# Optimization experiments

Hardware: AMD Instinct MI355X
Metric: run time of the kernel (lower is better)

The kernel has to match this reference:

```python
import jax, jax.numpy as jnp
import numpy as np

SEQ_LEN, BATCH, VOCAB, EMB, HID, NUM_LAYERS = 128, 64, 10000, 512, 512, 2


def setup_inputs() -> dict:
    key = jax.random.key(0)
    ks = jax.random.split(key, 16)
    b = float(np.sqrt(1.0 / HID))  # Linear init bound per init_weights_uniform
    u = lambda k, shape, bound: jax.random.uniform(k, shape, jnp.float32, -bound, bound)
    L = NUM_LAYERS - 1
    return {
        "inputs": jax.random.randint(ks[0], (SEQ_LEN, BATCH), 0, VOCAB, dtype=jnp.int32),
        "hidden": jnp.zeros((NUM_LAYERS, BATCH, HID), jnp.float32),
        "emb": u(ks[1], (VOCAB, EMB), 0.1),
        "W_ih0": u(ks[2], (HID, EMB), b),
        "b_ih0": u(ks[3], (HID,), b),
        "W_hh0": u(ks[4], (HID, HID), b),
        "b_hh0": u(ks[5], (HID,), b),
        "W_in": u(ks[6], (L, HID, HID), b),
        "b_in": u(ks[7], (L, HID), b),
        "W_hh": u(ks[8], (L, HID, HID), b),
        "b_hh": u(ks[9], (L, HID), b),
        "Wy": u(ks[10], (VOCAB, HID), 0.1),
        "by": jnp.zeros((VOCAB,), jnp.float32),
    }


def reference(inputs, hidden, emb, W_ih0, b_ih0, W_hh0, b_hh0,
              W_in, b_in, W_hh, b_hh, Wy, by):
    n_extra = W_in.shape[0]  # num_layers - 1 (static)

    def step(h, x_t):
        # h: [L, B, H]; x_t: [B] int tokens
        e = emb[x_t]  # [B, E]
        h0 = jnp.tanh(e @ W_ih0.T + b_ih0 + h[0] @ W_hh0.T + b_hh0)
        hs = [h0]
        for l in range(n_extra):  # small static layer loop
            hl = jnp.tanh(hs[-1] @ W_in[l].T + b_in[l]
                          + h[l + 1] @ W_hh[l].T + b_hh[l])
            hs.append(hl)
        h_new = jnp.stack(hs)  # [L, B, H]
        logits_t = hs[-1] @ Wy.T + by  # [B, V]
        return h_new, logits_t

    hidden_final, logits = jax.lax.scan(step, hidden, inputs)
    return logits, hidden_final  # [S, B, V], [L, B, H]
```

## Files before the change

### kernel.cpp

```cpp
#include <hip/hip_runtime.h>
#include <hip/hip_bf16.h>

#define SEQ 128
#define BAT 64
#define VOC 10000
#define EMBD 512
#define HID 512
#define BH (BAT*HID)
#define PRE0_OFF 0
#define H0_OFF   ((size_t)SEQ*BH)
#define H1_OFF   (H0_OFF + (size_t)(SEQ+1)*BH)
#define FLAGS_OFF (H1_OFF + (size_t)(SEQ+1)*BH)
#define CONV_OFF (FLAGS_OFF + 256)
#define LOGITS_N ((size_t)SEQ*BAT*VOC)
#define CONV_USHORTS 5382144ull
#define WS_NEED_FLOATS (CONV_OFF + CONV_USHORTS/2)

typedef __attribute__((ext_vector_type(8))) __bf16 bf16x8;
typedef __attribute__((ext_vector_type(4))) float f32x4;

__global__ __launch_bounds__(256) void init_state_k(const float* __restrict__ hidden,
                                                    float* __restrict__ h0_0,
                                                    float* __restrict__ h1_0,
                                                    unsigned* __restrict__ flags) {
    int i = blockIdx.x * 256 + threadIdx.x;
    if (i < 256) flags[i] = 0u;
    if (i < BH) { h0_0[i] = hidden[i]; h1_0[i] = hidden[BH + i]; }
}

__global__ __launch_bounds__(256) void gemm_nt_k(
    const float* __restrict__ A, const int* __restrict__ tok,
    const float* __restrict__ Bm,
    const float* __restrict__ bias0, const float* __restrict__ bias1,
    float* __restrict__ C, int N, int K, int ldc)
{
    __shared__ float As[32][132];
    __shared__ float Bs[32][132];
    __shared__ int toks[128];

    const int tid = threadIdx.x;
    const int r0 = blockIdx.x * 128;
    const int c0 = blockIdx.y * 128;

    if (tok != nullptr && tid < 128) toks[tid] = tok[r0 + tid];
    __syncthreads();

    const int tn = tid & 15;
    const int tm = tid >> 4;
    const int m0 = tm * 8, n0 = tn * 8;

    float acc[8][8];
#pragma unroll
    for (int i = 0; i < 8; ++i)
#pragma unroll
        for (int j = 0; j < 8; ++j) acc[i][j] = 0.f;

    for (int k0 = 0; k0 < K; k0 += 32) {
#pragma unroll
        for (int p = 0; p < 4; ++p) {
            int idx = p * 256 + tid;
            int row = idx >> 3;
            int kq  = (idx & 7) << 2;
            size_t arow = tok ? (size_t)toks[row] : (size_t)(r0 + row);
            float4 a = *(const float4*)(A + arow * (size_t)K + k0 + kq);
            As[kq+0][row] = a.x; As[kq+1][row] = a.y;
            As[kq+2][row] = a.z; As[kq+3][row] = a.w;
            int gc = c0 + row;
            float4 b = make_float4(0.f, 0.f, 0.f, 0.f);
            if (gc < N) b = *(const float4*)(Bm + (size_t)gc * K + k0 + kq);
            Bs[kq+0][row] = b.x; Bs[kq+1][row] = b.y;
            Bs[kq+2][row] = b.z; Bs[kq+3][row] = b.w;
        }
        __syncthreads();
#pragma unroll 8
        for (int k = 0; k < 32; ++k) {
            float4 a0 = *(const float4*)&As[k][m0];
            float4 a1 = *(const float4*)&As[k][m0 + 4];
            float4 b0 = *(const float4*)&Bs[k][n0];
            float4 b1 = *(const float4*)&Bs[k][n0 + 4];
            float am[8] = {a0.x,a0.y,a0.z,a0.w,a1.x,a1.y,a1.z,a1.w};
            float bn[8] = {b0.x,b0.y,b0.z,b0.w,b1.x,b1.y,b1.z,b1.w};
#pragma unroll
            for (int i = 0; i < 8; ++i)
#pragma unroll
                for (int j = 0; j < 8; ++j) acc[i][j] += am[i] * bn[j];
        }
        __syncthreads();
    }

    const bool full = (c0 + 128 <= N);
#pragma unroll
    for (int i = 0; i < 8; ++i) {
        size_t r = (size_t)(r0 + m0 + i);
        float* crow = C + r * (size_t)ldc;
#pragma unroll
        for (int j = 0; j < 8; ++j) {
            int c = c0 + n0 + j;
            if (full || c < N) {
                float v = acc[i][j];
                if (bias0) v += bias0[c];
                if (bias1) v += bias1[c];
                crow[c] = v;
            }
        }
    }
}


#define BFLY(S, N)                                                     \
    {                                                                  \
        _Pragma("unroll")                                              \
        for (int i = 0; i < N; ++i) {                                  \
            float lo_ = a[i], hi_ = a[i + N];                          \
            float send_ = (lane & S) ? lo_ : hi_;                      \
            float recv_ = __shfl_xor(send_, S);                        \
            a[i] = ((lane & S) ? hi_ : lo_) + recv_;                   \
        }                                                              \
    }

__global__ __launch_bounds__(512) void recurrence_k(
    const float* __restrict__ pre0, const float* __restrict__ W_hh0,
    const float* __restrict__ W_in, const float* __restrict__ b_in,
    const float* __restrict__ W_hh, const float* __restrict__ b_hh,
    float* __restrict__ h0_all, float* __restrict__ h1_all,
    unsigned* __restrict__ flags)
{
    __shared__ float xs[16384];

    const int tid  = threadIdx.x;
    const int lane = tid & 63;
    const int wv   = tid >> 6;
    const int p = ((lane&1)<<5)|((lane&2)<<3)|((lane&4)<<1)
                | ((lane&8)>>1)|((lane&16)>>3)|((lane&32)>>5);
    const int b_own = p >> 3, j_own = p & 7;

    unsigned* fl1 = flags;
    unsigned* fl2 = flags + 64;

    float4 wr[8][2];
    float a[64];

    if (blockIdx.x < 64) {
        const int g = blockIdx.x >> 4, jb = blockIdx.x & 15;
        const int bt = wv & 1, jt = wv >> 1;
        const size_t win = (size_t)(g << 4) * HID;
#pragma unroll
        for (int jj = 0; jj < 8; ++jj) {
            const float* wp = W_hh0 + (size_t)(jb*32 + jt*8 + jj) * HID;
            wr[jj][0] = *(const float4*)(wp + lane*4);
            wr[jj][1] = *(const float4*)(wp + 256 + lane*4);
        }
        const unsigned* grp = fl1 + (g << 4);
        unsigned* myf = fl1 + (g << 4) + jb;
        const int bg = (g << 4) + (bt << 3) + b_own;
        const int jg = jb*32 + jt*8 + j_own;

        for (unsigned t = 1; t <= SEQ; ++t) {
            float pf = pre0[(size_t)(t-1)*BH + (size_t)bg*HID + jg];
            for (;;) {
                unsigned v = __hip_atomic_load(&grp[lane & 15], __ATOMIC_RELAXED,
                                               __HIP_MEMORY_SCOPE_AGENT);
                if (__ballot(v < (t - 1)) == 0ull) break;
            }
            __syncthreads();
            {
                const float4* src = (const float4*)(h0_all + (size_t)(t-1)*BH + win);
                float4 r0_, r1_, r2_, r3_;
                asm volatile("global_load_dwordx4 %0, %1, off sc0 sc1" : "=v"(r0_) : "v"(src + tid));
                asm volatile("global_load_dwordx4 %0, %1, off sc0 sc1" : "=v"(r1_) : "v"(src + tid + 512));
                asm volatile("global_load_dwordx4 %0, %1, off sc0 sc1" : "=v"(r2_) : "v"(src + tid + 1024));
                asm volatile("global_load_dwordx4 %0, %1, off sc0 sc1" : "=v"(r3_) : "v"(src + tid + 1536));
                asm volatile("s_waitcnt vmcnt(0)" ::: "memory");
                __builtin_amdgcn_sched_barrier(0);
                float4* dst = (float4*)xs;
                dst[tid] = r0_; dst[tid+512] = r1_; dst[tid+1024] = r2_; dst[tid+1536] = r3_;
            }
            __syncthreads();
#pragma unroll
            for (int i = 0; i < 64; ++i) a[i] = 0.f;
#pragma unroll
            for (int b = 0; b < 8; ++b) {
                const int row = (bt << 3) + b;
                float4 ha = *(const float4*)&xs[row*512 + lane*4];
                float4 hb = *(const float4*)&xs[row*512 + 256 + lane*4];
#pragma unroll
                for (int jj = 0; jj < 8; ++jj) {
                    a[b*8+jj] += ha.x*wr[jj][0].x + ha.y*wr[jj][0].y
                               + ha.z*wr[jj][0].z + ha.w*wr[jj][0].w
                               + hb.x*wr[jj][1].x + hb.y*wr[jj][1].y
                               + hb.z*wr[jj][1].z + hb.w*wr[jj][1].w;
                }
            }
            BFLY(1,32) BFLY(2,16) BFLY(4,8) BFLY(8,4) BFLY(16,2) BFLY(32,1)
            float v = tanhf(a[0] + pf);
            __hip_atomic_store(&h0_all[(size_t)t*BH + (size_t)bg*HID + jg], v,
                               __ATOMIC_RELAXED, __HIP_MEMORY_SCOPE_AGENT);
            asm volatile("s_waitcnt vmcnt(0)" ::: "memory");
            __syncthreads();
            if (tid == 0) __hip_atomic_store(myf, t, __ATOMIC_RELAXED,
                                             __HIP_MEMORY_SCOPE_AGENT);
        }
    } else {
        const int idx = blockIdx.x - 64;
        const int g = idx >> 5, jb = idx & 31;
        const int bt = wv & 1, jt = (wv >> 1) & 1, kt = wv >> 2;
        const size_t win = (size_t)(g << 4) * HID;
        const float* Wmat = kt ? W_hh : W_in;
#pragma unroll
        for (int jj = 0; jj < 8; ++jj) {
            const float* wp = Wmat + (size_t)(jb*16 + jt*8 + jj) * HID;
            wr[jj][0] = *(const float4*)(wp + lane*4);
            wr[jj][1] = *(const float4*)(wp + 256 + lane*4);
        }
        const unsigned* grpA = fl1 + (g << 4);
        const unsigned* grpB = fl2 + (g << 5);
        unsigned* myf = fl2 + (g << 5) + jb;
        const int bg = (g << 4) + (bt << 3) + b_own;
        const int jg = jb*16 + jt*8 + j_own;
        const float bias = b_in[jg] + b_hh[jg];
        const int scx = (wv & 3) * 64 + lane;

        for (unsigned t = 1; t <= SEQ; ++t) {
            for (;;) {
                unsigned v1 = __hip_atomic_load(&grpA[lane & 15], __ATOMIC_RELAXED,
                                                __HIP_MEMORY_SCOPE_AGENT);
                unsigned v2 = __hip_atomic_load(&grpB[lane & 31], __ATOMIC_RELAXED,
                                                __HIP_MEMORY_SCOPE_AGENT);
                if (__ballot(v1 < t) == 0ull && __ballot(v2 < (t - 1)) == 0ull) break;
            }
            __syncthreads();
            {
                const int q = tid & 255;
                const float4* src = (tid < 256)
                    ? (const float4*)(h0_all + (size_t)t*BH + win)
                    : (const float4*)(h1_all + (size_t)(t-1)*BH + win);
                float4 rr[8];
#pragma unroll
                for (int i = 0; i < 8; ++i)
                    asm volatile("global_load_dwordx4 %0, %1, off sc0 sc1"
                                 : "=v"(rr[i]) : "v"(src + q + i*256));
                asm volatile("s_waitcnt vmcnt(0)" ::: "memory");
                __builtin_amdgcn_sched_barrier(0);
                float4* dst = (float4*)(xs + ((tid < 256) ? 0 : 8192));
#pragma unroll
                for (int i = 0; i < 8; ++i) dst[q + i*256] = rr[i];
            }
            __syncthreads();
#pragma unroll
            for (int i = 0; i < 64; ++i) a[i] = 0.f;
            const float* xsrc = xs + (kt ? 8192 : 0);
#pragma unroll
            for (int b = 0; b < 8; ++b) {
                const int row = (bt << 3) + b;
                float4 ha = *(const float4*)&xsrc[row*512 + lane*4];
                float4 hb = *(const float4*)&xsrc[row*512 + 256 + lane*4];
#pragma unroll
                for (int jj = 0; jj < 8; ++jj) {
                    a[b*8+jj] += ha.x*wr[jj][0].x + ha.y*wr[jj][0].y
                               + ha.z*wr[jj][0].z + ha.w*wr[jj][0].w
                               + hb.x*wr[jj][1].x + hb.y*wr[jj][1].y
                               + hb.z*wr[jj][1].z + hb.w*wr[jj][1].w;
                }
            }
            BFLY(1,32) BFLY(2,16) BFLY(4,8) BFLY(8,4) BFLY(16,2) BFLY(32,1)
            __syncthreads();
            if (kt) xs[scx] = a[0];
            __syncthreads();
            if (!kt) {
                float v = tanhf(a[0] + xs[scx] + bias);
                __hip_atomic_store(&h1_all[(size_t)t*BH + (size_t)bg*HID + jg], v,
                                   __ATOMIC_RELAXED, __HIP_MEMORY_SCOPE_AGENT);
            }
            asm volatile("s_waitcnt vmcnt(0)" ::: "memory");
            __syncthreads();
            if (tid == 0) __hip_atomic_store(myf, t, __ATOMIC_RELAXED,
                                             __HIP_MEMORY_SCOPE_AGENT);
        }
    }
}

__global__ __launch_bounds__(256) void copy_out_k(const float* __restrict__ h0_all,
                                                  const float* __restrict__ h1_all,
                                                  float* __restrict__ out_hidden) {
    int g = blockIdx.x * 256 + threadIdx.x;
    if (g < BH)            out_hidden[g] = h0_all[(size_t)SEQ * BH + g];
    else if (g < 2 * BH)   out_hidden[g] = h1_all[(size_t)SEQ * BH + (g - BH)];
}


__device__ __forceinline__ unsigned bf16_rne(float x) {
    unsigned u = __float_as_uint(x);
    unsigned r = u + 0x7fffu + ((u >> 16) & 1u);
    return r >> 16;
}

__global__ __launch_bounds__(256) void split_hi_k(const float* __restrict__ src,
                                                  unsigned short* __restrict__ hi,
                                                  int n4) {
    int i = blockIdx.x * 256 + threadIdx.x;
    if (i >= n4) return;
    float4 v = ((const float4*)src)[i];
    ushort4 h4;
    h4.x = (unsigned short)bf16_rne(v.x); h4.y = (unsigned short)bf16_rne(v.y);
    h4.z = (unsigned short)bf16_rne(v.z); h4.w = (unsigned short)bf16_rne(v.w);
    ((ushort4*)hi)[i] = h4;
}

__global__ __launch_bounds__(256) void gemm_mfma2f_k(
    const float* __restrict__ Ag, const int* __restrict__ tok,
    const unsigned short* __restrict__ Bhg,
    const float* __restrict__ bias0, const float* __restrict__ bias1,
    float* __restrict__ C, int N, int ldc)
{
    __shared__ __align__(16) unsigned short sAh[128*64];
    __shared__ __align__(16) unsigned short sAl[128*64];
    __shared__ __align__(16) unsigned short sBh[128*64];

    const int tid = threadIdx.x;
    const int flat = blockIdx.y * gridDim.x + blockIdx.x;
    const int cpx  = (gridDim.x * gridDim.y) >> 3;
    const int w    = (flat & 7) * cpx + (flat >> 3);
    const int r0 = (w & 63) * 128, c0 = (w >> 6) * 128;

    const int lane = tid & 63, wvv = tid >> 6;
    const int mh = wvv >> 1, nh = wvv & 1;

    f32x4 acc[4][4];
#pragma unroll
    for (int i = 0; i < 4; ++i)
#pragma unroll
        for (int j = 0; j < 4; ++j) acc[i][j] = (f32x4){0.f, 0.f, 0.f, 0.f};

    const int srow = tid >> 1, shalf = tid & 1;
    const size_t arow = tok ? (size_t)tok[r0 + srow] : (size_t)(r0 + srow);
    const size_t abase = arow * 512 + (size_t)shalf * 32;
    const int brow = c0 + srow;
    const bool bok = brow < N;
    const size_t bbase = (size_t)(bok ? brow : 0) * 512 + shalf * 32;
    const int woff = srow * 64;
    const int swz = srow & 7;

    float4 fa[4][2];
    uint4 vbh[4];
#pragma unroll
    for (int g = 0; g < 4; ++g) {
        fa[g][0] = *(const float4*)(Ag + abase + g*8);
        fa[g][1] = *(const float4*)(Ag + abase + g*8 + 4);
        vbh[g]   = bok ? *(const uint4*)(Bhg + bbase + g*8) : (uint4){0,0,0,0};
    }

    for (int k0 = 0; k0 < 512; k0 += 64) {
        __syncthreads();
#pragma unroll
        for (int g = 0; g < 4; ++g) {
            float f[8] = {fa[g][0].x, fa[g][0].y, fa[g][0].z, fa[g][0].w,
                          fa[g][1].x, fa[g][1].y, fa[g][1].z, fa[g][1].w};
            unsigned hh[8], ll[8];
#pragma unroll
            for (int q = 0; q < 8; ++q) {
                hh[q] = bf16_rne(f[q]);
                ll[q] = bf16_rne(f[q] - __uint_as_float(hh[q] << 16));
            }
            uint4 ph = { hh[0] | (hh[1]<<16), hh[2] | (hh[3]<<16),
                         hh[4] | (hh[5]<<16), hh[6] | (hh[7]<<16) };
            uint4 pl = { ll[0] | (ll[1]<<16), ll[2] | (ll[3]<<16),
                         ll[4] | (ll[5]<<16), ll[6] | (ll[7]<<16) };
            int off = woff + (((shalf*4 + g) ^ swz) * 8);
            *(uint4*)&sAh[off] = ph;
            *(uint4*)&sAl[off] = pl;
            *(uint4*)&sBh[off] = vbh[g];
        }
        __syncthreads();
        if (k0 < 448) {
            const int kn = k0 + 64;
#pragma unroll
            for (int g = 0; g < 4; ++g) {
                fa[g][0] = *(const float4*)(Ag + abase + kn + g*8);
                fa[g][1] = *(const float4*)(Ag + abase + kn + g*8 + 4);
                vbh[g]   = bok ? *(const uint4*)(Bhg + bbase + kn + g*8) : (uint4){0,0,0,0};
            }
        }
#pragma unroll
        for (int c = 0; c < 2; ++c) {
            const int ks = ((c*4 + (lane >> 4)) ^ (lane & 7)) * 8;
            bf16x8 fAh[4], fAl[4], fBh[4];
#pragma unroll
            for (int mi = 0; mi < 4; ++mi) {
                int ro = (mh*64 + mi*16 + (lane & 15)) * 64;
                fAh[mi] = *(const bf16x8*)&sAh[ro + ks];
                fAl[mi] = *(const bf16x8*)&sAl[ro + ks];
            }
#pragma unroll
            for (int ni = 0; ni < 4; ++ni) {
                int ro = (nh*64 + ni*16 + (lane & 15)) * 64;
                fBh[ni] = *(const bf16x8*)&sBh[ro + ks];
            }
#pragma unroll
            for (int mi = 0; mi < 4; ++mi)
#pragma unroll
                for (int ni = 0; ni < 4; ++ni) {
                    acc[mi][ni] = __builtin_amdgcn_mfma_f32_16x16x32_bf16(
                        fAh[mi], fBh[ni], acc[mi][ni], 0, 0, 0);
                    acc[mi][ni] = __builtin_amdgcn_mfma_f32_16x16x32_bf16(
                        fAl[mi], fBh[ni], acc[mi][ni], 0, 0, 0);
                }
        }
    }

#pragma unroll
    for (int ni = 0; ni < 4; ++ni) {
        int gcol = c0 + nh*64 + ni*16 + (lane & 15);
        bool ok = gcol < N;
        float bias = 0.f;
        if (ok) {
            if (bias0) bias += bias0[gcol];
            if (bias1) bias += bias1[gcol];
        }
#pragma unroll
        for (int mi = 0; mi < 4; ++mi) {
            int grow = r0 + mh*64 + mi*16 + ((lane >> 4) << 2);
#pragma unroll
            for (int r = 0; r < 4; ++r)
                if (ok) C[(size_t)(grow + r) * ldc + gcol] = acc[mi][ni][r] + bias;
        }
    }
}

extern "C" void kernel_launch(void* const* d_in, const int* in_sizes, int n_in,
                              void* d_out, int out_size, void* d_ws, size_t ws_size,
                              hipStream_t stream) {
    const int*   inputs = (const int*)d_in[0];
    const float* hidden = (const float*)d_in[1];
    const float* emb    = (const float*)d_in[2];
    const float* W_ih0  = (const float*)d_in[3];
    const float* b_ih0  = (const float*)d_in[4];
    const float* W_hh0  = (const float*)d_in[5];
    const float* b_hh0  = (const float*)d_in[6];
    const float* W_in   = (const float*)d_in[7];
    const float* b_in   = (const float*)d_in[8];
    const float* W_hh   = (const float*)d_in[9];
    const float* b_hh   = (const float*)d_in[10];
    const float* Wy     = (const float*)d_in[11];
    const float* by     = (const float*)d_in[12];
    float* out = (float*)d_out;

    float* ws     = (float*)d_ws;
    float* pre0   = ws + PRE0_OFF;
    float* h0_all = ws + H0_OFF;
    float* h1_all = ws + H1_OFF;
    unsigned* flags = (unsigned*)(ws + FLAGS_OFF);
    float* out_hidden = out + LOGITS_N;
    const bool big_ws = (ws_size >= WS_NEED_FLOATS * 4ull);

    unsigned short* wy_hi   = (unsigned short*)(ws + CONV_OFF);
    unsigned short* wih0_hi = wy_hi + (size_t)VOC * HID;

    init_state_k<<<dim3((BH + 255) / 256), dim3(256), 0, stream>>>(hidden, h0_all, h1_all, flags);

    if (big_ws) {
        split_hi_k<<<dim3(1024), dim3(256), 0, stream>>>(W_ih0, wih0_hi, HID*EMBD/4);
        split_hi_k<<<dim3(5000), dim3(256), 0, stream>>>(Wy, wy_hi, VOC*HID/4);
        gemm_mfma2f_k<<<dim3(64, 4), dim3(256), 0, stream>>>(
            emb, inputs, wih0_hi, b_ih0, b_hh0, pre0, HID, HID);
    } else {
        gemm_nt_k<<<dim3(64, 4), dim3(256), 0, stream>>>(
            emb, inputs, W_ih0, b_ih0, b_hh0, pre0, HID, EMBD, HID);
    }

    const float* pre0_c = pre0;
    void* kargs[] = { (void*)&pre0_c, (void*)&W_hh0, (void*)&W_in, (void*)&b_in,
                      (void*)&W_hh, (void*)&b_hh, (void*)&h0_all, (void*)&h1_all,
                      (void*)&flags };
    hipLaunchCooperativeKernel((const void*)recurrence_k, dim3(192), dim3(512),
                               kargs, 0, stream);

    copy_out_k<<<dim3(256), dim3(256), 0, stream>>>(h0_all, h1_all, out_hidden);

    if (big_ws) {
        gemm_mfma2f_k<<<dim3(64, 79), dim3(256), 0, stream>>>(
            h1_all + BH, nullptr, wy_hi, by, nullptr, out, VOC, VOC);
    } else {
        gemm_nt_k<<<dim3(64, 79), dim3(256), 0, stream>>>(
            h1_all + BH, nullptr, Wy, nullptr, by, out, VOC, HID, VOC);
    }
}
```

Baseline: 1.233 ms.

## Add finer-grained flag-synchronized recurrence kernel with per-group dependencies

Adds a new cooperative recurrence kernel that splits layers across separate blocks (128 per layer, 256 blocks of 256 threads). Each wave polls only the flags of its batch group instead of relying on a block-wide barrier, so layer 1 can pipeline behind layer 0 at a finer granularity. Hidden states are read through cache-bypassing loads and published with per-wave release flags. The aim is to cut synchronization latency on the sequential critical path, at the cost of more flag traffic, spin polling, and an occupancy-dependent fallback to the old kernel.

```diff
diff --git a/kernel.cpp b/kernel.cpp
--- a/kernel.cpp
+++ b/kernel.cpp
@@ -11,7 +11,7 @@
 #define H0_OFF   ((size_t)SEQ*BH)
 #define H1_OFF   (H0_OFF + (size_t)(SEQ+1)*BH)
 #define FLAGS_OFF (H1_OFF + (size_t)(SEQ+1)*BH)
-#define CONV_OFF (FLAGS_OFF + 256)
+#define CONV_OFF (FLAGS_OFF + 2048)
 #define LOGITS_N ((size_t)SEQ*BAT*VOC)
 #define CONV_USHORTS 5382144ull
 #define WS_NEED_FLOATS (CONV_OFF + CONV_USHORTS/2)
@@ -24,7 +24,7 @@
                                                     float* __restrict__ h1_0,
                                                     unsigned* __restrict__ flags) {
     int i = blockIdx.x * 256 + threadIdx.x;
-    if (i < 256) flags[i] = 0u;
+    if (i < 2048) flags[i] = 0u;
     if (i < BH) { h0_0[i] = hidden[i]; h1_0[i] = hidden[BH + i]; }
 }
 
@@ -106,14 +106,13 @@
     }
 }
 
-
 #define BFLY(S, N)                                                     \
     {                                                                  \
         _Pragma("unroll")                                              \
         for (int i = 0; i < N; ++i) {                                  \
             float lo_ = a[i], hi_ = a[i + N];                          \
             float send_ = (lane & S) ? lo_ : hi_;                      \
-            float recv_ = __shfl_xor(send_, S);                        \
+            float recv_ = __shfl_xor(send_, S);                       \
             a[i] = ((lane & S) ? hi_ : lo_) + recv_;                   \
         }                                                              \
     }
@@ -275,6 +274,146 @@
             __syncthreads();
             if (tid == 0) __hip_atomic_store(myf, t, __ATOMIC_RELAXED,
                                              __HIP_MEMORY_SCOPE_AGENT);
+        }
+    }
+}
+
+__global__ __launch_bounds__(256) void recurrence6_k(
+    const float* __restrict__ pre0, const float* __restrict__ W_hh0,
+    const float* __restrict__ W_in, const float* __restrict__ b_in,
+    const float* __restrict__ W_hh, const float* __restrict__ b_hh,
+    float* __restrict__ h0_all, float* __restrict__ h1_all,
+    unsigned* __restrict__ flags)
+{
+    const int tid  = threadIdx.x;
+    const int lane = tid & 63;
+    const int wv   = tid >> 6;
+    const int bt = wv & 1, jt = wv >> 1;
+    const int p = ((lane&1)<<5)|((lane&2)<<3)|((lane&4)<<1)
+                | ((lane&8)>>1)|((lane&16)>>3)|((lane&32)>>5);
+    const int layer = blockIdx.x >> 7;
+    const int idx = blockIdx.x & 127;
+    const int g = idx >> 5, jb = idx & 31;
+    const int b_st = (g << 4) + (bt << 3) + (p >> 3);
+    const int j_st = (jb << 4) + (jt << 3) + (p & 7);
+
+    unsigned* fl1 = flags + (g << 7);
+    unsigned* fl2 = flags + 512 + (g << 7);
+    const unsigned* poll1 = fl1 + (bt << 6);
+    const unsigned* poll2 = fl2 + (bt << 6);
+    unsigned* myf = (layer ? fl2 : fl1) + (bt << 6) + (jb << 1) + jt;
+
+    const size_t rowbase = (size_t)((g << 4) + (bt << 3)) * HID;
+    float a[64];
+    float4 xa[8], xc[8];
+
+    if (layer == 0) {
+        const float* wbase = W_hh0 + (size_t)((jb << 4) + (jt << 3)) * HID;
+        for (unsigned t = 1; t <= SEQ; ++t) {
+            float pf = pre0[(size_t)(t-1)*BH + (size_t)b_st*HID + j_st];
+            for (;;) {
+                unsigned v = __hip_atomic_load(&poll1[lane], __ATOMIC_RELAXED,
+                                               __HIP_MEMORY_SCOPE_AGENT);
+                if (__ballot(v < t - 1) == 0ull) break;
+            }
+            const float* xb = h0_all + (size_t)(t-1)*BH + rowbase;
+#pragma unroll
+            for (int r = 0; r < 8; ++r) {
+                const float4* pa = (const float4*)(xb + r*HID) + lane;
+                const float4* pb = (const float4*)(xb + r*HID + 256) + lane;
+                asm volatile("global_load_dwordx4 %0, %1, off sc0 sc1" : "=v"(xa[r]) : "v"(pa));
+                asm volatile("global_load_dwordx4 %0, %1, off sc0 sc1" : "=v"(xc[r]) : "v"(pb));
+            }
+            asm volatile("s_waitcnt vmcnt(0)" ::: "memory");
+            __builtin_amdgcn_sched_barrier(0);
+#pragma unroll
+            for (int i = 0; i < 64; ++i) a[i] = 0.f;
+#pragma unroll
+            for (int jj = 0; jj < 8; ++jj) {
+                const float* wp = wbase + (size_t)jj * HID;
+                float4 w0 = *(const float4*)(wp + (lane << 2));
+                float4 w1 = *(const float4*)(wp + 256 + (lane << 2));
+#pragma unroll
+                for (int r = 0; r < 8; ++r)
+                    a[(r<<3)+jj] += xa[r].x*w0.x + xa[r].y*w0.y
+                                  + xa[r].z*w0.z + xa[r].w*w0.w
+                                  + xc[r].x*w1.x + xc[r].y*w1.y
+                                  + xc[r].z*w1.z + xc[r].w*w1.w;
+            }
+            BFLY(1,32) BFLY(2,16) BFLY(4,8) BFLY(8,4) BFLY(16,2) BFLY(32,1)
+            float v = tanhf(a[0] + pf);
+            __hip_atomic_store(&h0_all[(size_t)t*BH + (size_t)b_st*HID + j_st], v,
+                               __ATOMIC_RELAXED, __HIP_MEMORY_SCOPE_AGENT);
+            if (lane == 0) __hip_atomic_store(myf, t, __ATOMIC_RELEASE,
+                                              __HIP_MEMORY_SCOPE_AGENT);
+        }
+    } else {
+        const float* wibase = W_in + (size_t)((jb << 4) + (jt << 3)) * HID;
+        const float* whbase = W_hh + (size_t)((jb << 4) + (jt << 3)) * HID;
+        const float bias = b_in[j_st] + b_hh[j_st];
+        for (unsigned t = 1; t <= SEQ; ++t) {
+            for (;;) {
+                unsigned v = __hip_atomic_load(&poll1[lane], __ATOMIC_RELAXED,
+                                               __HIP_MEMORY_SCOPE_AGENT);
+                if (__ballot(v < t) == 0ull) break;
+            }
+            const float* xb0 = h0_all + (size_t)t*BH + rowbase;
+#pragma unroll
+            for (int r = 0; r < 8; ++r) {
+                const float4* pa = (const float4*)(xb0 + r*HID) + lane;
+                const float4* pb = (const float4*)(xb0 + r*HID + 256) + lane;
+                asm volatile("global_load_dwordx4 %0, %1, off sc0 sc1" : "=v"(xa[r]) : "v"(pa));
+                asm volatile("global_load_dwordx4 %0, %1, off sc0 sc1" : "=v"(xc[r]) : "v"(pb));
+            }
+            asm volatile("s_waitcnt vmcnt(0)" ::: "memory");
+            __builtin_amdgcn_sched_barrier(0);
+#pragma unroll
+            for (int i = 0; i < 64; ++i) a[i] = 0.f;
+#pragma unroll
+            for (int jj = 0; jj < 8; ++jj) {
+                const float* wp = wibase + (size_t)jj * HID;
+                float4 w0 = *(const float4*)(wp + (lane << 2));
+                float4 w1 = *(const float4*)(wp + 256 + (lane << 2));
+#pragma unroll
+                for (int r = 0; r < 8; ++r)
+                    a[(r<<3)+jj] += xa[r].x*w0.x + xa[r].y*w0.y
+                                  + xa[r].z*w0.z + xa[r].w*w0.w
+                                  + xc[r].x*w1.x + xc[r].y*w1.y
+                                  + xc[r].z*w1.z + xc[r].w*w1.w;
+            }
+            for (;;) {
+                unsigned v = __hip_atomic_load(&poll2[lane], __ATOMIC_RELAXED,
+                                               __HIP_MEMORY_SCOPE_AGENT);
+                if (__ballot(v < t - 1) == 0ull) break;
+            }
+            const float* xb1 = h1_all + (size_t)(t-1)*BH + rowbase;
+#pragma unroll
+            for (int r = 0; r < 8; ++r) {
+                const float4* pa = (const float4*)(xb1 + r*HID) + lane;
+                const float4* pb = (const float4*)(xb1 + r*HID + 256) + lane;
+                asm volatile("global_load_dwordx4 %0, %1, off sc0 sc1" : "=v"(xa[r]) : "v"(pa));
+                asm volatile("global_load_dwordx4 %0, %1, off sc0 sc1" : "=v"(xc[r]) : "v"(pb));
+            }
+            asm volatile("s_waitcnt vmcnt(0)" ::: "memory");
+            __builtin_amdgcn_sched_barrier(0);
+#pragma unroll
+            for (int jj = 0; jj < 8; ++jj) {
+                const float* wp = whbase + (size_t)jj * HID;
+                float4 w0 = *(const float4*)(wp + (lane << 2));
+                float4 w1 = *(const float4*)(wp + 256 + (lane << 2));
+#pragma unroll
+                for (int r = 0; r < 8; ++r)
+                    a[(r<<3)+jj] += xa[r].x*w0.x + xa[r].y*w0.y
+                                  + xa[r].z*w0.z + xa[r].w*w0.w
+                                  + xc[r].x*w1.x + xc[r].y*w1.y
+                                  + xc[r].z*w1.z + xc[r].w*w1.w;
+            }
+            BFLY(1,32) BFLY(2,16) BFLY(4,8) BFLY(8,4) BFLY(16,2) BFLY(32,1)
+            float v = tanhf(a[0] + bias);
+            __hip_atomic_store(&h1_all[(size_t)t*BH + (size_t)b_st*HID + j_st], v,
+                               __ATOMIC_RELAXED, __HIP_MEMORY_SCOPE_AGENT);
+            if (lane == 0) __hip_atomic_store(myf, t, __ATOMIC_RELEASE,
+                                              __HIP_MEMORY_SCOPE_AGENT);
         }
     }
 }
@@ -448,14 +587,15 @@
     float* pre0   = ws + PRE0_OFF;
     float* h0_all = ws + H0_OFF;
     float* h1_all = ws + H1_OFF;
-    unsigned* flags = (unsigned*)(ws + FLAGS_OFF);
+    unsigned* flags4 = (unsigned*)(ws + FLAGS_OFF);
+    unsigned* flags6 = flags4 + 256;
     float* out_hidden = out + LOGITS_N;
     const bool big_ws = (ws_size >= WS_NEED_FLOATS * 4ull);
 
     unsigned short* wy_hi   = (unsigned short*)(ws + CONV_OFF);
     unsigned short* wih0_hi = wy_hi + (size_t)VOC * HID;
 
-    init_state_k<<<dim3((BH + 255) / 256), dim3(256), 0, stream>>>(hidden, h0_all, h1_all, flags);
+    init_state_k<<<dim3((BH + 255) / 256), dim3(256), 0, stream>>>(hidden, h0_all, h1_all, flags4);
 
     if (big_ws) {
         split_hi_k<<<dim3(1024), dim3(256), 0, stream>>>(W_ih0, wih0_hi, HID*EMBD/4);
@@ -468,11 +608,26 @@
     }
 
     const float* pre0_c = pre0;
-    void* kargs[] = { (void*)&pre0_c, (void*)&W_hh0, (void*)&W_in, (void*)&b_in,
-                      (void*)&W_hh, (void*)&b_hh, (void*)&h0_all, (void*)&h1_all,
-                      (void*)&flags };
-    hipLaunchCooperativeKernel((const void*)recurrence_k, dim3(192), dim3(512),
-                               kargs, 0, stream);
+    void* kargs6[] = { (void*)&pre0_c, (void*)&W_hh0, (void*)&W_in, (void*)&b_in,
+                       (void*)&W_hh, (void*)&b_hh, (void*)&h0_all, (void*)&h1_all,
+                       (void*)&flags6 };
+    void* kargs4[] = { (void*)&pre0_c, (void*)&W_hh0, (void*)&W_in, (void*)&b_in,
+                       (void*)&W_hh, (void*)&b_hh, (void*)&h0_all, (void*)&h1_all,
+                       (void*)&flags4 };
+    int nb = 0;
+    hipError_t oe = hipOccupancyMaxActiveBlocksPerMultiprocessor(
+        &nb, (const void*)recurrence6_k, 256, 0);
+    bool done = false;
+    if (oe == hipSuccess && nb >= 1) {
+        hipError_t e = hipLaunchCooperativeKernel((const void*)recurrence6_k,
+                                                  dim3(256), dim3(256), kargs6, 0, stream);
+        if (e == hipSuccess) done = true;
+        else (void)hipGetLastError();
+    }
+    if (!done) {
+        hipLaunchCooperativeKernel((const void*)recurrence_k, dim3(192), dim3(512),
+                                   kargs4, 0, stream);
+    }
 
     copy_out_k<<<dim3(256), dim3(256), 0, stream>>>(h0_all, h1_all, out_hidden);
 
```

Result: slower. 3.145 ms (+155.1%).
